# Optimization experiments

Hardware: AMD Instinct MI355X
Metric: run time of the kernel (lower is better)

Reference implementation:

```python
import jax, jax.numpy as jnp
import numpy as np

B, L, NE, DOUT = 4, 4096, 64, 64
DI = 128          # backbone model dim (hardcoded d_inner in MambaDoc)
NL = 2            # num_layers
H = 2             # num_heads
N = 128           # state_dim
G = 1             # num_groups
CONV = 4          # conv_size
DIN = 2 * DI      # expand=2 -> 256 inner channels of the mixer
P = DIN // H      # headdim = 128
CCH = DIN + 2 * G * N      # 512 conv channels (x, B, C)
DPROJ = 2 * DIN + 2 * G * N + H  # 770 in_proj output width


def setup_inputs() -> dict:
    key = jax.random.key(0)
    ks = jax.random.split(key, 8)
    s = lambda k, shape, sc: (jax.random.normal(k, shape, jnp.float32) * sc)
    return {
        "x": s(ks[0], (B, L, NE), 1.0),
        "in_w": s(ks[1], (DI, NE), (1.0 / NE) ** 0.5),
        "in_b": jnp.zeros((DI,), jnp.float32),
        "out_w": s(ks[2], (DOUT, DI), (1.0 / DI) ** 0.5),
        "out_b": jnp.zeros((DOUT,), jnp.float32),
        "l_rms_w": jnp.ones((NL, DI), jnp.float32),
        "l_in_w": s(ks[3], (NL, DPROJ, DI), (1.0 / DI) ** 0.5),
        "conv_w": s(ks[4], (NL, CCH, CONV), (1.0 / CONV) ** 0.5),
        "conv_b": jnp.zeros((NL, CCH), jnp.float32),
        "dt_bias": s(ks[5], (NL, H), 0.1),
        "A_log": jnp.zeros((NL, H), jnp.float32),   # A = -exp(A_log) = -1
        "D_p": jnp.ones((NL, H), jnp.float32),
        "gnorm_w": jnp.ones((NL, DIN), jnp.float32),
        "l_out_w": s(ks[6], (NL, DI, DIN), (1.0 / DIN) ** 0.5),
        "fnorm_w": jnp.ones((DI,), jnp.float32),
    }


def _rms(x, w, eps=1e-5):
    return x * jax.lax.rsqrt(jnp.mean(x * x, -1, keepdims=True) + eps) * w


def _mamba_layer(x, rms_w, in_w, cw, cb, dtb, a_log, d, gnw, ow):
    # x: (B,L,DI)
    h = _rms(x, rms_w)
    zxbcdt = jnp.einsum("bld,ed->ble", h, in_w)  # (B,L,770)
    z, xBC, dt = jnp.split(zxbcdt, [DIN, DIN + CCH], axis=-1)
    # causal depthwise conv over time, conv_size taps
    xp = jnp.pad(xBC, ((0, 0), (CONV - 1, 0), (0, 0)))
    xc = cb + sum(xp[:, k:k + L, :] * cw[:, k] for k in range(CONV))
    xc = jax.nn.silu(xc)
    xs, Bm, Cm = jnp.split(xc, [DIN, DIN + G * N], axis=-1)
    xs = xs.reshape(B, L, H, P)
    dt = jax.nn.softplus(dt + dtb)                 # (B,L,H)
    dA = jnp.exp(dt * (-jnp.exp(a_log)))           # (B,L,H) discrete decay

    def step(hc, inp):
        dA_t, dt_t, x_t, B_t, C_t = inp  # (B,H),(B,H),(B,H,P),(B,N),(B,N)
        hc = hc * dA_t[:, :, None, None] + (dt_t[:, :, None] * x_t)[..., None] * B_t[:, None, None, :]
        y = jnp.einsum("bhpn,bn->bhp", hc, C_t)
        return hc, y

    h0 = jnp.zeros((B, H, P, N), x.dtype)
    seq = (jnp.moveaxis(dA, 1, 0), jnp.moveaxis(dt, 1, 0), jnp.moveaxis(xs, 1, 0),
           jnp.moveaxis(Bm, 1, 0), jnp.moveaxis(Cm, 1, 0))
    _, ys = jax.lax.scan(step, h0, seq)
    y = jnp.moveaxis(ys, 0, 1)                     # (B,L,H,P)
    y = y + xs * d[None, None, :, None]            # D skip connection
    y = _rms(y.reshape(B, L, DIN) * jax.nn.silu(z), gnw)  # gated RMSNorm
    return x + jnp.einsum("ble,de->bld", y, ow)


def reference(x, in_w, in_b, out_w, out_b, l_rms_w, l_in_w, conv_w, conv_b,
              dt_bias, A_log, D_p, gnorm_w, l_out_w, fnorm_w):
    xp = jnp.einsum("bln,dn->bld", x, in_w) + in_b
    h = xp
    for i in range(NL):
        h = _mamba_layer(h, l_rms_w[i], l_in_w[i], conv_w[i], conv_b[i],
                         dt_bias[i], A_log[i], D_p[i], gnorm_w[i], l_out_w[i])
    h = _rms(h, fnorm_w)            # backbone final norm
    out = xp + h                    # outer residual in MambaDoc.forward
    return jnp.einsum("bld,od->blo", out, out_w) + out_b
```

## Files before the change

### kernel.cpp

```cpp
#include <hip/hip_runtime.h>
#include <cstddef>
#include <cstdint>


#define LSEQ 4096
#define MTOK 16384

typedef unsigned short u16;
typedef _Float16 f16x8 __attribute__((ext_vector_type(8)));
typedef float f32x4 __attribute__((ext_vector_type(4)));

__device__ __forceinline__ u16 f2h(float x) {
    return __builtin_bit_cast(u16, (_Float16)x);
}
__device__ __forceinline__ float h2f(u16 u) {
    return (float)__builtin_bit_cast(_Float16, u);
}
__device__ __forceinline__ float silu_f(float x) { return x / (1.f + __expf(-x)); }

__device__ __forceinline__ void async_lds16(const void* g, void* l) {
    __builtin_amdgcn_global_load_lds(
        (const __attribute__((address_space(1))) unsigned int*)g,
        (__attribute__((address_space(3))) unsigned int*)l, 16, 0, 0);
}

__device__ __forceinline__ uint4 cvt8(const float* __restrict__ src) {
    float4 a = *(const float4*)src;
    float4 b = *(const float4*)(src + 4);
    union { u16 u[8]; uint4 q; } pk;
    pk.u[0] = f2h(a.x); pk.u[1] = f2h(a.y); pk.u[2] = f2h(a.z); pk.u[3] = f2h(a.w);
    pk.u[4] = f2h(b.x); pk.u[5] = f2h(b.y); pk.u[6] = f2h(b.z); pk.u[7] = f2h(b.w);
    return pk.q;
}

__global__ __launch_bounds__(256) void gemm_rms0_kernel(
    const float* __restrict__ xf, const float* __restrict__ wf,
    const float* __restrict__ bias, const float* __restrict__ rmsw,
    u16* __restrict__ xp16, u16* __restrict__ hbuf16, u16* __restrict__ hn16)
{
    __shared__ u16 sA[64 * 64];
    __shared__ u16 sW[128 * 64];
    __shared__ float red[64][33];
    __shared__ float srstd[64];
    const int m0 = blockIdx.y * 64;
    const int tid = threadIdx.x, wid = tid >> 6, lane = tid & 63;
    const int wm = (wid >> 1) * 32, wn = (wid & 1) * 64;
    const int quad = lane >> 4, cl = lane & 15;
    #pragma unroll
    for (int i = 0; i < 2; i++) {
        int ck = i * 256 + tid;
        int r = ck >> 3, cc = ck & 7;
        int csw = (cc ^ (r & 7)) << 3;
        *(uint4*)&sA[ck * 8] = cvt8(xf + (size_t)(m0 + r) * 64 + csw);
    }
    #pragma unroll
    for (int i = 0; i < 4; i++) {
        int ck = i * 256 + tid;
        int r = ck >> 3, cc = ck & 7;
        int csw = (cc ^ (r & 7)) << 3;
        *(uint4*)&sW[ck * 8] = cvt8(wf + (size_t)r * 64 + csw);
    }
    __syncthreads();
    f32x4 acc[2][4];
    #pragma unroll
    for (int i = 0; i < 2; i++)
        #pragma unroll
        for (int j = 0; j < 4; j++) acc[i][j] = f32x4{0.f, 0.f, 0.f, 0.f};
    #pragma unroll
    for (int ks = 0; ks < 2; ks++) {
        f16x8 af[2], wv[4];
        int kc = ks * 4 + quad;
        #pragma unroll
        for (int i = 0; i < 2; i++) {
            int r = wm + i * 16 + cl;
            af[i] = *(const f16x8*)&sA[r * 64 + ((kc ^ (r & 7)) << 3)];
        }
        #pragma unroll
        for (int j = 0; j < 4; j++) {
            int r = wn + j * 16 + cl;
            wv[j] = *(const f16x8*)&sW[r * 64 + ((kc ^ (r & 7)) << 3)];
        }
        #pragma unroll
        for (int i = 0; i < 2; i++)
            #pragma unroll
            for (int j = 0; j < 4; j++)
                acc[i][j] = __builtin_amdgcn_mfma_f32_16x16x32_f16(
                    af[i], wv[j], acc[i][j], 0, 0, 0);
    }
    const int slot = (wid & 1) * 16 + cl;
    #pragma unroll
    for (int i = 0; i < 2; i++)
        #pragma unroll
        for (int r = 0; r < 4; r++) {
            int t = wm + i * 16 + quad * 4 + r;
            float ssp = 0.f;
            #pragma unroll
            for (int j = 0; j < 4; j++) {
                int n = wn + j * 16 + cl;
                float v = acc[i][j][r] + bias[n];
                acc[i][j][r] = v;
                ssp += v * v;
            }
            red[t][slot] = ssp;
        }
    __syncthreads();
    if (tid < 64) {
        float s = 0.f;
        #pragma unroll
        for (int sl = 0; sl < 32; sl++) s += red[tid][sl];
        srstd[tid] = rsqrtf(s * (1.f / 128.f) + 1e-5f);
    }
    __syncthreads();
    #pragma unroll
    for (int i = 0; i < 2; i++)
        #pragma unroll
        for (int r = 0; r < 4; r++) {
            int t = wm + i * 16 + quad * 4 + r;
            size_t ob = (size_t)(m0 + t) * 128;
            float rstd = srstd[t];
            #pragma unroll
            for (int j = 0; j < 4; j++) {
                int n = wn + j * 16 + cl;
                float v = acc[i][j][r];
                u16 vh = f2h(v);
                xp16[ob + n] = vh;
                hbuf16[ob + n] = vh;
                hn16[ob + n] = f2h(v * rstd * rmsw[n]);
            }
        }
}

__global__ __launch_bounds__(256) void gemm_inproj_kernel(
    const u16* __restrict__ A, const float* __restrict__ Wf,
    u16* __restrict__ zx16, float* __restrict__ dtb, float* __restrict__ Sb,
    const float* __restrict__ dt_bias, const float* __restrict__ A_log)
{
    __shared__ u16 sA[128 * 64];
    __shared__ u16 sW[128 * 64];
    __shared__ float sdt[2][128];
    const int K = 128, N = 770;
    const int n0 = blockIdx.x * 128, m0 = blockIdx.y * 128;
    const int tid = threadIdx.x, wid = tid >> 6, lane = tid & 63;
    const int wm = (wid >> 1) * 64, wn = (wid & 1) * 64;
    const int quad = lane >> 4, cl = lane & 15;
    f32x4 acc[4][4];
    #pragma unroll
    for (int i = 0; i < 4; i++)
        #pragma unroll
        for (int j = 0; j < 4; j++) acc[i][j] = f32x4{0.f, 0.f, 0.f, 0.f};

    for (int k0 = 0; k0 < K; k0 += 64) {
        #pragma unroll
        for (int i = 0; i < 4; i++) {
            int ck = i * 256 + tid;
            int r = ck >> 3, cc = ck & 7;
            int csw = (cc ^ (r & 7)) << 3;
            async_lds16(A + (size_t)(m0 + r) * K + k0 + csw,
                        (void*)(sA + (i * 256 + (tid & ~63)) * 8));
        }
        #pragma unroll
        for (int i = 0; i < 4; i++) {
            int ck = i * 256 + tid;
            int r = ck >> 3, cc = ck & 7;
            int csw = (cc ^ (r & 7)) << 3;
            int rr = n0 + r; if (rr >= N) rr = N - 1;
            *(uint4*)&sW[ck * 8] = cvt8(Wf + (size_t)rr * K + k0 + csw);
        }
        __syncthreads();
        #pragma unroll
        for (int ks = 0; ks < 2; ks++) {
            f16x8 af[4], wv[4];
            int kc = ks * 4 + quad;
            #pragma unroll
            for (int i = 0; i < 4; i++) {
                int r = wm + i * 16 + cl;
                af[i] = *(const f16x8*)&sA[r * 64 + ((kc ^ (r & 7)) << 3)];
            }
            #pragma unroll
            for (int j = 0; j < 4; j++) {
                int r = wn + j * 16 + cl;
                wv[j] = *(const f16x8*)&sW[r * 64 + ((kc ^ (r & 7)) << 3)];
            }
            #pragma unroll
            for (int i = 0; i < 4; i++)
                #pragma unroll
                for (int j = 0; j < 4; j++)
                    acc[i][j] = __builtin_amdgcn_mfma_f32_16x16x32_f16(
                        af[i], wv[j], acc[i][j], 0, 0, 0);
        }
        __syncthreads();
    }
    if (blockIdx.x < 6) {
        #pragma unroll
        for (int i = 0; i < 4; i++) {
            int m = m0 + wm + i * 16 + quad * 4;
            #pragma unroll
            for (int j = 0; j < 4; j++) {
                int n = n0 + wn + j * 16 + cl;
                #pragma unroll
                for (int r = 0; r < 4; r++)
                    zx16[(size_t)(m + r) * 768 + n] = f2h(acc[i][j][r]);
            }
        }
    } else {
        if ((wid & 1) == 0 && cl < 2) {
            #pragma unroll
            for (int i = 0; i < 4; i++)
                #pragma unroll
                for (int r = 0; r < 4; r++)
                    sdt[cl][wm + i * 16 + quad * 4 + r] = acc[i][0][r];
        }
        __syncthreads();
        const int hh = tid >> 7, t = tid & 127;
        float raw = sdt[hh][t] + dt_bias[hh];
        float dt = fmaxf(raw, 0.f) + log1pf(__expf(-fabsf(raw)));
        dtb[(size_t)(m0 + t) * 2 + hh] = dt;
        float ad = -__expf(A_log[hh]) * dt;
        __syncthreads();
        sdt[hh][t] = ad;
        __syncthreads();
        for (int off = 1; off < 128; off <<= 1) {
            float add = (t >= off) ? sdt[hh][t - off] : 0.f;
            __syncthreads();
            sdt[hh][t] += add;
            __syncthreads();
        }
        Sb[(size_t)(m0 + t) * 2 + hh] = sdt[hh][t];
    }
}

__global__ __launch_bounds__(512) void chunkstate_conv_kernel(
    const u16* __restrict__ zx16, const float* __restrict__ cw,
    const float* __restrict__ cb, const float* __restrict__ dtb,
    const float* __restrict__ Sb, u16* __restrict__ xT, u16* __restrict__ Hb)
{
    __shared__ u16 raw[2560 * 8];
    __shared__ u16 XT[128 * 128];
    __shared__ u16 BT[128 * 128];
    __shared__ float scw[2][128][4];
    __shared__ float scb[2][128];
    __shared__ float ssw[128];
    const int c = blockIdx.x, h = blockIdx.y, b = blockIdx.z;
    const int tid = threadIdx.x, wid = tid >> 6, lane = tid & 63;
    const int quad = lane >> 4, cl = lane & 15;
    const int tok0 = b * LSEQ + c * 128;
    for (int idx = tid; idx < 256; idx += 512) {
        int grp = idx >> 7, j = idx & 127;
        int ch = grp ? (256 + j) : (128 * h + j);
        float4 w4 = *(const float4*)&cw[ch * 4];
        scw[grp][j][0] = w4.x; scw[grp][j][1] = w4.y;
        scw[grp][j][2] = w4.z; scw[grp][j][3] = w4.w;
        scb[grp][j] = cb[ch];
    }
    if (tid < 128) {
        float Sl = Sb[(size_t)(tok0 + 127) * 2 + h];
        ssw[tid] = __expf(Sl - Sb[(size_t)(tok0 + tid) * 2 + h])
                   * dtb[(size_t)(tok0 + tid) * 2 + h];
    }
    #pragma unroll
    for (int i = 0; i < 5; i++) {
        int ck = i * 512 + tid;
        int r = ck >> 4; if (r > 130) r = 130;
        int cc = ck & 15;
        int tok = tok0 - 3 + r; if (tok < 0) tok = 0;
        async_lds16(zx16 + (size_t)tok * 768 + 256 + 128 * h + ((cc ^ (r & 15)) << 3),
                    (void*)(raw + (i * 512 + (tid & ~63)) * 8));
    }
    __syncthreads();
    if (c == 0 && tid < 48) *(uint4*)&raw[tid * 8] = make_uint4(0, 0, 0, 0);
    __syncthreads();
    #pragma unroll
    for (int it = 0; it < 4; it++) {
        int idx = it * 512 + tid;
        int s = idx & 127, pg = idx >> 7;
        f16x8 v[4];
        #pragma unroll
        for (int k = 0; k < 4; k++) {
            int rr = s + k;
            v[k] = *(const f16x8*)&raw[rr * 128 + ((pg ^ (rr & 15)) << 3)];
        }
        #pragma unroll
        for (int j = 0; j < 8; j++) {
            int p = pg * 8 + j;
            float o = scb[0][p] + (float)v[0][j] * scw[0][p][0]
                    + (float)v[1][j] * scw[0][p][1]
                    + (float)v[2][j] * scw[0][p][2]
                    + (float)v[3][j] * scw[0][p][3];
            o = silu_f(o);
            XT[p * 128 + (((s >> 3) ^ (p & 15)) << 3) + (s & 7)] = f2h(o);
        }
    }
    __syncthreads();
    const size_t blk = ((size_t)((b * 2 + h) * 32 + c)) << 14;
    #pragma unroll
    for (int i = 0; i < 5; i++) {
        int ck = i * 512 + tid;
        int r = ck >> 4; if (r > 130) r = 130;
        int cc = ck & 15;
        int tok = tok0 - 3 + r; if (tok < 0) tok = 0;
        async_lds16(zx16 + (size_t)tok * 768 + 512 + ((cc ^ (r & 15)) << 3),
                    (void*)(raw + (i * 512 + (tid & ~63)) * 8));
    }
    #pragma unroll
    for (int it = 0; it < 4; it++) {
        int ck = it * 512 + tid;
        int r = ck >> 4, cc = ck & 15;
        uint4 q = *(const uint4*)&XT[r * 128 + ((cc ^ (r & 15)) << 3)];
        *(uint4*)&xT[blk + (size_t)r * 128 + cc * 8] = q;
    }
    __syncthreads();
    if (c == 0 && tid < 48) *(uint4*)&raw[tid * 8] = make_uint4(0, 0, 0, 0);
    __syncthreads();
    #pragma unroll
    for (int it = 0; it < 4; it++) {
        int idx = it * 512 + tid;
        int s = idx & 127, ng = idx >> 7;
        f16x8 v[4];
        #pragma unroll
        for (int k = 0; k < 4; k++) {
            int rr = s + k;
            v[k] = *(const f16x8*)&raw[rr * 128 + ((ng ^ (rr & 15)) << 3)];
        }
        float wsv = ssw[s];
        #pragma unroll
        for (int j = 0; j < 8; j++) {
            int n = ng * 8 + j;
            float o = scb[1][n] + (float)v[0][j] * scw[1][n][0]
                    + (float)v[1][j] * scw[1][n][1]
                    + (float)v[2][j] * scw[1][n][2]
                    + (float)v[3][j] * scw[1][n][3];
            o = silu_f(o) * wsv;
            BT[n * 128 + (((s >> 3) ^ (n & 15)) << 3) + (s & 7)] = f2h(o);
        }
    }
    __syncthreads();
    const int wm = (wid >> 1) * 32, wn = (wid & 1) * 64;
    f32x4 acc[2][4];
    #pragma unroll
    for (int i = 0; i < 2; i++)
        #pragma unroll
        for (int j = 0; j < 4; j++) acc[i][j] = f32x4{0.f, 0.f, 0.f, 0.f};
    #pragma unroll
    for (int ks = 0; ks < 4; ks++) {
        f16x8 xa[2], bb[4];
        int kc = ks * 4 + quad;
        #pragma unroll
        for (int i = 0; i < 2; i++) {
            int r = wm + i * 16 + cl;
            xa[i] = *(const f16x8*)&XT[r * 128 + ((kc ^ (r & 15)) << 3)];
        }
        #pragma unroll
        for (int j = 0; j < 4; j++) {
            int r = wn + j * 16 + cl;
            bb[j] = *(const f16x8*)&BT[r * 128 + ((kc ^ (r & 15)) << 3)];
        }
        #pragma unroll
        for (int i = 0; i < 2; i++)
            #pragma unroll
            for (int j = 0; j < 4; j++)
                acc[i][j] = __builtin_amdgcn_mfma_f32_16x16x32_f16(
                    xa[i], bb[j], acc[i][j], 0, 0, 0);
    }
    u16* out = Hb + blk;
    #pragma unroll
    for (int i = 0; i < 2; i++)
        #pragma unroll
        for (int j = 0; j < 4; j++)
            #pragma unroll
            for (int r = 0; r < 4; r++)
                out[(size_t)(wm + i * 16 + quad * 4 + r) * 128 + wn + j * 16 + cl]
                    = f2h(acc[i][j][r]);
}

__global__ __launch_bounds__(256) void statecombine_kernel(
    const float* __restrict__ Sb, const u16* __restrict__ Hb,
    u16* __restrict__ Hbf)
{
    const int e = blockIdx.x * 256 + threadIdx.x;
    const int h = blockIdx.y, b = blockIdx.z;
    const size_t base = ((size_t)((b * 2 + h) * 32)) << 14;
    float state = 0.f;
    for (int c = 0; c < 32; c++) {
        size_t idx = base + ((size_t)c << 14) + e;
        float v = h2f(Hb[idx]);
        Hbf[idx] = f2h(state);
        float dec = __expf(Sb[(size_t)(b * LSEQ + c * 128 + 127) * 2 + h]);
        state = dec * state + v;
    }
}

__global__ __launch_bounds__(512) void ssd_fused_conv_kernel(
    const u16* __restrict__ zx16, const u16* __restrict__ xT,
    const u16* __restrict__ Hbf, const float* __restrict__ dtb,
    const float* __restrict__ Sb, const float* __restrict__ cw,
    const float* __restrict__ cb, const float* __restrict__ gnw,
    const float* __restrict__ Dp, u16* __restrict__ y16)
{
    __shared__ u16 bufCW[2][128 * 128];
    __shared__ u16 bufH[2][128 * 128];
    __shared__ float sS[2][128], sdt[2][128];
    __shared__ float scw2[2][128][4];
    __shared__ float scb2[2][128];
    __shared__ float red[128][5];
    __shared__ float srstd[128];
    const int c = blockIdx.x, b = blockIdx.y;
    const int tid = threadIdx.x, wid = tid >> 6, lane = tid & 63;
    const int quad = lane >> 4, cl = lane & 15;
    const int tok0 = b * LSEQ + c * 128;
    const size_t blk0 = ((size_t)((b * 2 + 0) * 32 + c)) << 14;
    const size_t blk1 = ((size_t)((b * 2 + 1) * 32 + c)) << 14;
    u16* scratch = &bufH[0][0];
    for (int idx = tid; idx < 256; idx += 512) {
        int grp = idx >> 7, j = idx & 127;
        int ch = grp ? (256 + j) : (384 + j);
        float4 w4 = *(const float4*)&cw[ch * 4];
        scw2[grp][j][0] = w4.x; scw2[grp][j][1] = w4.y;
        scw2[grp][j][2] = w4.z; scw2[grp][j][3] = w4.w;
        scb2[grp][j] = cb[ch];
    }
    if (tid < 256) {
        int hh = tid >> 7, t = tid & 127;
        sS[hh][t] = Sb[(size_t)(tok0 + t) * 2 + hh];
        sdt[hh][t] = dtb[(size_t)(tok0 + t) * 2 + hh];
    }
    #pragma unroll
    for (int i = 0; i < 5; i++) {
        int ck = i * 512 + tid;
        int r = ck >> 4; if (r > 130) r = 130;
        int cc = ck & 15;
        int tok = tok0 - 3 + r; if (tok < 0) tok = 0;
        async_lds16(zx16 + (size_t)tok * 768 + 640 + ((cc ^ (r & 15)) << 3),
                    (void*)(scratch + (i * 512 + (tid & ~63)) * 8));
    }
    __syncthreads();
    if (c == 0 && tid < 48) *(uint4*)&scratch[tid * 8] = make_uint4(0, 0, 0, 0);
    __syncthreads();
    #pragma unroll
    for (int it = 0; it < 4; it++) {
        int idx = it * 512 + tid;
        int t = idx & 127, ng = idx >> 7;
        f16x8 v[4];
        #pragma unroll
        for (int k = 0; k < 4; k++) {
            int rr = t + k;
            v[k] = *(const f16x8*)&scratch[rr * 128 + ((ng ^ (rr & 15)) << 3)];
        }
        union { u16 u[8]; uint4 q; } pk;
        #pragma unroll
        for (int j = 0; j < 8; j++) {
            int n = ng * 8 + j;
            float o = scb2[0][n] + (float)v[0][j] * scw2[0][n][0]
                    + (float)v[1][j] * scw2[0][n][1]
                    + (float)v[2][j] * scw2[0][n][2]
                    + (float)v[3][j] * scw2[0][n][3];
            pk.u[j] = f2h(silu_f(o));
        }
        *(uint4*)&bufCW[0][t * 128 + ((ng ^ (t & 15)) << 3)] = pk.q;
    }
    __syncthreads();
    #pragma unroll
    for (int i = 0; i < 5; i++) {
        int ck = i * 512 + tid;
        int r = ck >> 4; if (r > 130) r = 130;
        int cc = ck & 15;
        int tok = tok0 - 3 + r; if (tok < 0) tok = 0;
        async_lds16(zx16 + (size_t)tok * 768 + 512 + ((cc ^ (r & 15)) << 3),
                    (void*)(scratch + (i * 512 + (tid & ~63)) * 8));
    }
    __syncthreads();
    if (c == 0 && tid < 48) *(uint4*)&scratch[tid * 8] = make_uint4(0, 0, 0, 0);
    __syncthreads();
    #pragma unroll
    for (int it = 0; it < 4; it++) {
        int idx = it * 512 + tid;
        int t = idx & 127, ng = idx >> 7;
        f16x8 v[4];
        #pragma unroll
        for (int k = 0; k < 4; k++) {
            int rr = t + k;
            v[k] = *(const f16x8*)&scratch[rr * 128 + ((ng ^ (rr & 15)) << 3)];
        }
        union { u16 u[8]; uint4 q; } pk;
        #pragma unroll
        for (int j = 0; j < 8; j++) {
            int n = ng * 8 + j;
            float o = scb2[1][n] + (float)v[0][j] * scw2[1][n][0]
                    + (float)v[1][j] * scw2[1][n][1]
                    + (float)v[2][j] * scw2[1][n][2]
                    + (float)v[3][j] * scw2[1][n][3];
            pk.u[j] = f2h(silu_f(o));
        }
        *(uint4*)&bufCW[1][t * 128 + ((ng ^ (t & 15)) << 3)] = pk.q;
    }
    __syncthreads();
    #pragma unroll
    for (int i = 0; i < 4; i++) {
        int ck = i * 512 + tid;
        int r = ck >> 4, cc = ck & 15;
        int csw = (cc ^ (r & 15)) << 3;
        int ldst = (i * 512 + (tid & ~63)) * 8;
        async_lds16(Hbf + blk0 + (size_t)r * 128 + csw, (void*)(&bufH[0][0] + ldst));
        async_lds16(Hbf + blk1 + (size_t)r * 128 + csw, (void*)(&bufH[1][0] + ldst));
    }
    __syncthreads();
    const int h = wid >> 2, w2 = wid & 3;
    const int wm = (w2 >> 1) * 64, wn = (w2 & 1) * 64;
    f32x4 acc[4][4];
    #pragma unroll
    for (int i = 0; i < 4; i++)
        #pragma unroll
        for (int j = 0; j < 4; j++) acc[i][j] = f32x4{0.f, 0.f, 0.f, 0.f};
    #pragma unroll
    for (int ks = 0; ks < 4; ks++) {
        f16x8 ca[4], hb[4];
        int kc = ks * 4 + quad;
        #pragma unroll
        for (int i = 0; i < 4; i++) {
            int r = wm + i * 16 + cl;
            ca[i] = *(const f16x8*)&bufCW[0][r * 128 + ((kc ^ (r & 15)) << 3)];
        }
        #pragma unroll
        for (int j = 0; j < 4; j++) {
            int r = wn + j * 16 + cl;
            hb[j] = *(const f16x8*)&bufH[h][r * 128 + ((kc ^ (r & 15)) << 3)];
        }
        #pragma unroll
        for (int i = 0; i < 4; i++)
            #pragma unroll
            for (int j = 0; j < 4; j++)
                acc[i][j] = __builtin_amdgcn_mfma_f32_16x16x32_f16(
                    ca[i], hb[j], acc[i][j], 0, 0, 0);
    }
    #pragma unroll
    for (int i = 0; i < 4; i++)
        #pragma unroll
        for (int r = 0; r < 4; r++) {
            float e = __expf(sS[h][wm + i * 16 + quad * 4 + r]);
            #pragma unroll
            for (int j = 0; j < 4; j++) acc[i][j][r] *= e;
        }
    const int sm0 = (wid >> 1) * 32, sn0 = (wid & 1) * 64;
    f32x4 sacc[2][4];
    #pragma unroll
    for (int i = 0; i < 2; i++)
        #pragma unroll
        for (int j = 0; j < 4; j++) sacc[i][j] = f32x4{0.f, 0.f, 0.f, 0.f};
    #pragma unroll
    for (int ks = 0; ks < 4; ks++) {
        f16x8 cs[2], bs[4];
        int kc = ks * 4 + quad;
        #pragma unroll
        for (int i2 = 0; i2 < 2; i2++) {
            int r = sm0 + i2 * 16 + cl;
            cs[i2] = *(const f16x8*)&bufCW[0][r * 128 + ((kc ^ (r & 15)) << 3)];
        }
        #pragma unroll
        for (int j = 0; j < 4; j++) {
            int r = sn0 + j * 16 + cl;
            bs[j] = *(const f16x8*)&bufCW[1][r * 128 + ((kc ^ (r & 15)) << 3)];
        }
        #pragma unroll
        for (int i2 = 0; i2 < 2; i2++)
            #pragma unroll
            for (int j = 0; j < 4; j++)
                if (sm0 + i2 * 16 + 15 >= sn0 + j * 16)
                    sacc[i2][j] = __builtin_amdgcn_mfma_f32_16x16x32_f16(
                        cs[i2], bs[j], sacc[i2][j], 0, 0, 0);
    }
    __syncthreads();
    #pragma unroll
    for (int i = 0; i < 4; i++) {
        int ck = i * 512 + tid;
        int r = ck >> 4, cc = ck & 15;
        int csw = (cc ^ (r & 15)) << 3;
        int ldst = (i * 512 + (tid & ~63)) * 8;
        async_lds16(xT + blk0 + (size_t)r * 128 + csw, (void*)(&bufH[0][0] + ldst));
        async_lds16(xT + blk1 + (size_t)r * 128 + csw, (void*)(&bufH[1][0] + ldst));
    }
    #pragma unroll
    for (int hh = 0; hh < 2; hh++)
        #pragma unroll
        for (int i2 = 0; i2 < 2; i2++)
            #pragma unroll
            for (int r = 0; r < 4; r++) {
                int t = sm0 + i2 * 16 + quad * 4 + r;
                float Stv = sS[hh][t];
                #pragma unroll
                for (int j = 0; j < 4; j++) {
                    int s = sn0 + j * 16 + cl;
                    float gv = 0.f;
                    if (s <= t)
                        gv = sacc[i2][j][r] * __expf(Stv - sS[hh][s]) * sdt[hh][s];
                    bufCW[hh][t * 128 + (((s >> 3) ^ (t & 15)) << 3) + (s & 7)] = f2h(gv);
                }
            }
    __syncthreads();
    #pragma unroll
    for (int ks = 0; ks < 4; ks++) {
        f16x8 ga[4], xb[4];
        int kc = ks * 4 + quad;
        #pragma unroll
        for (int i = 0; i < 4; i++) {
            int r = wm + i * 16 + cl;
            ga[i] = *(const f16x8*)&bufCW[h][r * 128 + ((kc ^ (r & 15)) << 3)];
        }
        #pragma unroll
        for (int j = 0; j < 4; j++) {
            int r = wn + j * 16 + cl;
            xb[j] = *(const f16x8*)&bufH[h][r * 128 + ((kc ^ (r & 15)) << 3)];
        }
        #pragma unroll
        for (int i = 0; i < 4; i++)
            #pragma unroll
            for (int j = 0; j < 4; j++)
                acc[i][j] = __builtin_amdgcn_mfma_f32_16x16x32_f16(
                    ga[i], xb[j], acc[i][j], 0, 0, 0);
    }
    const float dco = Dp[h];
    #pragma unroll
    for (int i = 0; i < 4; i++)
        #pragma unroll
        for (int r = 0; r < 4; r++) {
            int t = wm + i * 16 + quad * 4 + r;
            float ssp = 0.f;
            #pragma unroll
            for (int j = 0; j < 4; j++) {
                int p = wn + j * 16 + cl;
                float xv = h2f(bufH[h][p * 128 + (((t >> 3) ^ (p & 15)) << 3) + (t & 7)]);
                float zv = h2f(zx16[(size_t)(tok0 + t) * 768 + h * 128 + p]);
                float g = (acc[i][j][r] + dco * xv) * silu_f(zv);
                acc[i][j][r] = g;
                ssp += g * g;
            }
            ssp += __shfl_xor(ssp, 1);
            ssp += __shfl_xor(ssp, 2);
            ssp += __shfl_xor(ssp, 4);
            ssp += __shfl_xor(ssp, 8);
            if (cl == 0) red[t][h * 2 + (wn >> 6)] = ssp;
        }
    __syncthreads();
    if (tid < 128)
        srstd[tid] = rsqrtf((red[tid][0] + red[tid][1] + red[tid][2] + red[tid][3])
                            * (1.f / 256.f) + 1e-5f);
    __syncthreads();
    #pragma unroll
    for (int i = 0; i < 4; i++)
        #pragma unroll
        for (int r = 0; r < 4; r++) {
            int t = wm + i * 16 + quad * 4 + r;
            float rstd = srstd[t];
            u16* row = y16 + (size_t)(tok0 + t) * 256;
            #pragma unroll
            for (int j = 0; j < 4; j++) {
                int p = wn + j * 16 + cl;
                int e = h * 128 + p;
                row[e] = f2h(acc[i][j][r] * rstd * gnw[e]);
            }
        }
}

__global__ __launch_bounds__(256) void gemm_outrms_kernel(
    const u16* __restrict__ A, const float* __restrict__ Wf,
    const float* __restrict__ rmsw, u16* __restrict__ xp16,
    u16* __restrict__ hbuf16, u16* __restrict__ hn16,
    const float* __restrict__ out_wf, const float* __restrict__ out_b,
    float* __restrict__ dout, int mode)
{
    __shared__ u16 sA[64 * 64];
    __shared__ u16 sW[128 * 64];
    __shared__ float red[64][33];
    __shared__ float srstd[64];
    __shared__ u16 hn2[64 * 128];
    __shared__ u16 ow[64 * 128];
    const int K = 256;
    const int m0 = blockIdx.y * 64;
    const int tid = threadIdx.x, wid = tid >> 6, lane = tid & 63;
    const int wm = (wid >> 1) * 32, wn = (wid & 1) * 64;
    const int quad = lane >> 4, cl = lane & 15;
    f32x4 acc[2][4];
    #pragma unroll
    for (int i = 0; i < 2; i++)
        #pragma unroll
        for (int j = 0; j < 4; j++) acc[i][j] = f32x4{0.f, 0.f, 0.f, 0.f};

    for (int k0 = 0; k0 < K; k0 += 64) {
        #pragma unroll
        for (int i = 0; i < 2; i++) {
            int ck = i * 256 + tid;
            int r = ck >> 3, cc = ck & 7;
            int csw = (cc ^ (r & 7)) << 3;
            async_lds16(A + (size_t)(m0 + r) * K + k0 + csw,
                        (void*)(sA + (i * 256 + (tid & ~63)) * 8));
        }
        #pragma unroll
        for (int i = 0; i < 4; i++) {
            int ck = i * 256 + tid;
            int r = ck >> 3, cc = ck & 7;
            int csw = (cc ^ (r & 7)) << 3;
            *(uint4*)&sW[ck * 8] = cvt8(Wf + (size_t)r * K + k0 + csw);
        }
        __syncthreads();
        #pragma unroll
        for (int ks = 0; ks < 2; ks++) {
            f16x8 af[2], wv[4];
            int kc = ks * 4 + quad;
            #pragma unroll
            for (int i = 0; i < 2; i++) {
                int r = wm + i * 16 + cl;
                af[i] = *(const f16x8*)&sA[r * 64 + ((kc ^ (r & 7)) << 3)];
            }
            #pragma unroll
            for (int j = 0; j < 4; j++) {
                int r = wn + j * 16 + cl;
                wv[j] = *(const f16x8*)&sW[r * 64 + ((kc ^ (r & 7)) << 3)];
            }
            #pragma unroll
            for (int i = 0; i < 2; i++)
                #pragma unroll
                for (int j = 0; j < 4; j++)
                    acc[i][j] = __builtin_amdgcn_mfma_f32_16x16x32_f16(
                        af[i], wv[j], acc[i][j], 0, 0, 0);
        }
        __syncthreads();
    }
    const int slot = (wid & 1) * 16 + cl;
    #pragma unroll
    for (int i = 0; i < 2; i++)
        #pragma unroll
        for (int r = 0; r < 4; r++) {
            int t = wm + i * 16 + quad * 4 + r;
            size_t ob = (size_t)(m0 + t) * 128;
            float ssp = 0.f;
            #pragma unroll
            for (int j = 0; j < 4; j++) {
                int n = wn + j * 16 + cl;
                float v = acc[i][j][r] + h2f(hbuf16[ob + n]);
                acc[i][j][r] = v;
                ssp += v * v;
            }
            red[t][slot] = ssp;
        }
    __syncthreads();
    if (tid < 64) {
        float s = 0.f;
        #pragma unroll
        for (int sl = 0; sl < 32; sl++) s += red[tid][sl];
        srstd[tid] = rsqrtf(s * (1.f / 128.f) + 1e-5f);
    }
    __syncthreads();
    #pragma unroll
    for (int i = 0; i < 2; i++)
        #pragma unroll
        for (int r = 0; r < 4; r++) {
            int t = wm + i * 16 + quad * 4 + r;
            size_t ob = (size_t)(m0 + t) * 128;
            float rstd = srstd[t];
            #pragma unroll
            for (int j = 0; j < 4; j++) {
                int n = wn + j * 16 + cl;
                float v = acc[i][j][r];
                float val = v * rstd * rmsw[n];
                if (mode == 1) {
                    hbuf16[ob + n] = f2h(v);
                    hn16[ob + n] = f2h(val);
                } else {
                    val += h2f(xp16[ob + n]);
                    hn2[t * 128 + (((n >> 3) ^ (t & 15)) << 3) + (n & 7)] = f2h(val);
                }
            }
        }
    if (mode == 1) return;
    #pragma unroll
    for (int i = 0; i < 4; i++) {
        int ck = i * 256 + tid;
        int rr = ck >> 4, cc = ck & 15;
        int csw = (cc ^ (rr & 15)) << 3;
        *(uint4*)&ow[ck * 8] = cvt8(out_wf + (size_t)rr * 128 + csw);
    }
    __syncthreads();
    const int wm4 = (wid >> 1) * 32, wn4 = (wid & 1) * 32;
    f32x4 acc2[2][2];
    #pragma unroll
    for (int i = 0; i < 2; i++)
        #pragma unroll
        for (int j = 0; j < 2; j++) acc2[i][j] = f32x4{0.f, 0.f, 0.f, 0.f};
    #pragma unroll
    for (int ks = 0; ks < 4; ks++) {
        f16x8 af2[2], wf2[2];
        int kc = ks * 4 + quad;
        #pragma unroll
        for (int i = 0; i < 2; i++) {
            int r = wm4 + i * 16 + cl;
            af2[i] = *(const f16x8*)&hn2[r * 128 + ((kc ^ (r & 15)) << 3)];
        }
        #pragma unroll
        for (int j = 0; j < 2; j++) {
            int rr = wn4 + j * 16 + cl;
            wf2[j] = *(const f16x8*)&ow[rr * 128 + ((kc ^ (rr & 15)) << 3)];
        }
        #pragma unroll
        for (int i = 0; i < 2; i++)
            #pragma unroll
            for (int j = 0; j < 2; j++)
                acc2[i][j] = __builtin_amdgcn_mfma_f32_16x16x32_f16(
                    af2[i], wf2[j], acc2[i][j], 0, 0, 0);
    }
    #pragma unroll
    for (int i = 0; i < 2; i++) {
        int m = m0 + wm4 + i * 16 + quad * 4;
        #pragma unroll
        for (int j = 0; j < 2; j++) {
            int n = wn4 + j * 16 + cl;
            float bv = out_b[n];
            #pragma unroll
            for (int r = 0; r < 4; r++)
                dout[(size_t)(m + r) * 64 + n] = acc2[i][j][r] + bv;
        }
    }
}

extern "C" void kernel_launch(void* const* d_in, const int* in_sizes, int n_in,
                              void* d_out, int out_size, void* d_ws, size_t ws_size,
                              hipStream_t stream)
{
    (void)in_sizes; (void)n_in; (void)out_size; (void)ws_size;
    const float* x       = (const float*)d_in[0];
    const float* in_w    = (const float*)d_in[1];
    const float* in_b    = (const float*)d_in[2];
    const float* out_w   = (const float*)d_in[3];
    const float* out_b   = (const float*)d_in[4];
    const float* l_rms_w = (const float*)d_in[5];
    const float* l_in_w  = (const float*)d_in[6];
    const float* conv_w  = (const float*)d_in[7];
    const float* conv_b  = (const float*)d_in[8];
    const float* dt_bias = (const float*)d_in[9];
    const float* A_log   = (const float*)d_in[10];
    const float* D_p     = (const float*)d_in[11];
    const float* gnorm_w = (const float*)d_in[12];
    const float* l_out_w = (const float*)d_in[13];
    const float* fnorm_w = (const float*)d_in[14];

    char* w = (char*)d_ws;
    u16*   xp16   = (u16*)(w);
    u16*   hbuf16 = (u16*)(w + 4194304);
    u16*   hn16   = (u16*)(w + 8388608);
    u16*   zx16   = (u16*)(w + 12582912);
    float* dtb    = (float*)(w + 37748736);
    float* Sb     = (float*)(w + 37879808);
    u16*   Hb     = (u16*)(w + 38010880);
    u16*   Hbf    = (u16*)(w + 46399488);
    u16*   xT     = (u16*)(w + 54788096);
    u16*   y16    = (u16*)(w + 63176704);

    gemm_rms0_kernel<<<dim3(1, 256), 256, 0, stream>>>(
        x, in_w, in_b, l_rms_w, xp16, hbuf16, hn16);

    for (int i = 0; i < 2; i++) {
        gemm_inproj_kernel<<<dim3(7, 128), 256, 0, stream>>>(
            hn16, l_in_w + (size_t)i * 770 * 128, zx16, dtb, Sb,
            dt_bias + i * 2, A_log + i * 2);
        chunkstate_conv_kernel<<<dim3(32, 2, 4), 512, 0, stream>>>(
            zx16, conv_w + i * 2048, conv_b + i * 512, dtb, Sb, xT, Hb);
        statecombine_kernel<<<dim3(64, 2, 4), 256, 0, stream>>>(Sb, Hb, Hbf);
        ssd_fused_conv_kernel<<<dim3(32, 4), 512, 0, stream>>>(
            zx16, xT, Hbf, dtb, Sb, conv_w + i * 2048, conv_b + i * 512,
            gnorm_w + i * 256, D_p + i * 2, y16);
        gemm_outrms_kernel<<<dim3(1, 256), 256, 0, stream>>>(
            y16, l_out_w + (size_t)i * 128 * 256,
            (i == 0) ? (l_rms_w + 128) : fnorm_w, xp16, hbuf16, hn16,
            out_w, out_b, (float*)d_out, (i == 0) ? 1 : 3);
    }
}
```

Measured before the change: 246.2 us.

## Split SSD kernel per head and move gated RMSNorm into out-proj GEMM

The SSD output kernel now launches one block per (chunk, head, batch) instead of per (chunk, batch), which doubles the grid to 256 blocks. Each block recomputes the x-channel conv for its own head instead of reading a stored xT buffer, so the chunkstate kernel no longer writes xT. Because a single block no longer holds both heads, the cross-head gated RMSNorm moves into the out-projection GEMM. That kernel first computes the per-row rstd from the un-normalized gated output, folds gnorm_w into the weight conversion, and scales the accumulator by rstd. The trade is extra conv recomputation and an extra pass over the 256-wide row in the out GEMM, in exchange for more parallelism and less global traffic.

```diff
diff --git a/kernel.cpp b/kernel.cpp
--- a/kernel.cpp
+++ b/kernel.cpp
@@ -30,6 +30,20 @@
     union { u16 u[8]; uint4 q; } pk;
     pk.u[0] = f2h(a.x); pk.u[1] = f2h(a.y); pk.u[2] = f2h(a.z); pk.u[3] = f2h(a.w);
     pk.u[4] = f2h(b.x); pk.u[5] = f2h(b.y); pk.u[6] = f2h(b.z); pk.u[7] = f2h(b.w);
+    return pk.q;
+}
+
+__device__ __forceinline__ uint4 cvt8g(const float* __restrict__ src,
+                                       const float* __restrict__ gw) {
+    float4 a = *(const float4*)src;
+    float4 b = *(const float4*)(src + 4);
+    float4 ga = *(const float4*)gw;
+    float4 gb = *(const float4*)(gw + 4);
+    union { u16 u[8]; uint4 q; } pk;
+    pk.u[0] = f2h(a.x * ga.x); pk.u[1] = f2h(a.y * ga.y);
+    pk.u[2] = f2h(a.z * ga.z); pk.u[3] = f2h(a.w * ga.w);
+    pk.u[4] = f2h(b.x * gb.x); pk.u[5] = f2h(b.y * gb.y);
+    pk.u[6] = f2h(b.z * gb.z); pk.u[7] = f2h(b.w * gb.w);
     return pk.q;
 }
 
@@ -232,7 +246,7 @@
 __global__ __launch_bounds__(512) void chunkstate_conv_kernel(
     const u16* __restrict__ zx16, const float* __restrict__ cw,
     const float* __restrict__ cb, const float* __restrict__ dtb,
-    const float* __restrict__ Sb, u16* __restrict__ xT, u16* __restrict__ Hb)
+    const float* __restrict__ Sb, u16* __restrict__ Hb)
 {
     __shared__ u16 raw[2560 * 8];
     __shared__ u16 XT[128 * 128];
@@ -291,7 +305,6 @@
         }
     }
     __syncthreads();
-    const size_t blk = ((size_t)((b * 2 + h) * 32 + c)) << 14;
     #pragma unroll
     for (int i = 0; i < 5; i++) {
         int ck = i * 512 + tid;
@@ -300,13 +313,6 @@
         int tok = tok0 - 3 + r; if (tok < 0) tok = 0;
         async_lds16(zx16 + (size_t)tok * 768 + 512 + ((cc ^ (r & 15)) << 3),
                     (void*)(raw + (i * 512 + (tid & ~63)) * 8));
-    }
-    #pragma unroll
-    for (int it = 0; it < 4; it++) {
-        int ck = it * 512 + tid;
-        int r = ck >> 4, cc = ck & 15;
-        uint4 q = *(const uint4*)&XT[r * 128 + ((cc ^ (r & 15)) << 3)];
-        *(uint4*)&xT[blk + (size_t)r * 128 + cc * 8] = q;
     }
     __syncthreads();
     if (c == 0 && tid < 48) *(uint4*)&raw[tid * 8] = make_uint4(0, 0, 0, 0);
@@ -334,6 +340,7 @@
         }
     }
     __syncthreads();
+    const size_t blk = ((size_t)((b * 2 + h) * 32 + c)) << 14;
     const int wm = (wid >> 1) * 32, wn = (wid & 1) * 64;
     f32x4 acc[2][4];
     #pragma unroll
@@ -389,40 +396,104 @@
     }
 }
 
-__global__ __launch_bounds__(512) void ssd_fused_conv_kernel(
-    const u16* __restrict__ zx16, const u16* __restrict__ xT,
-    const u16* __restrict__ Hbf, const float* __restrict__ dtb,
-    const float* __restrict__ Sb, const float* __restrict__ cw,
-    const float* __restrict__ cb, const float* __restrict__ gnw,
-    const float* __restrict__ Dp, u16* __restrict__ y16)
+__global__ __launch_bounds__(512) void ssd_ph_kernel(
+    const u16* __restrict__ zx16, const u16* __restrict__ Hbf,
+    const float* __restrict__ dtb, const float* __restrict__ Sb,
+    const float* __restrict__ cw, const float* __restrict__ cb,
+    const float* __restrict__ Dp, u16* __restrict__ g16)
 {
-    __shared__ u16 bufCW[2][128 * 128];
-    __shared__ u16 bufH[2][128 * 128];
-    __shared__ float sS[2][128], sdt[2][128];
-    __shared__ float scw2[2][128][4];
-    __shared__ float scb2[2][128];
-    __shared__ float red[128][5];
-    __shared__ float srstd[128];
-    const int c = blockIdx.x, b = blockIdx.y;
+    __shared__ u16 raw[2560 * 8];
+    __shared__ u16 XT[128 * 128];
+    __shared__ u16 Btok[128 * 128];
+    __shared__ u16 Ctok[128 * 128];
+    __shared__ float sS[128], sdt[128];
+    __shared__ float scw[3][128][4];
+    __shared__ float scb[3][128];
+    const int c = blockIdx.x, h = blockIdx.y, b = blockIdx.z;
     const int tid = threadIdx.x, wid = tid >> 6, lane = tid & 63;
     const int quad = lane >> 4, cl = lane & 15;
     const int tok0 = b * LSEQ + c * 128;
-    const size_t blk0 = ((size_t)((b * 2 + 0) * 32 + c)) << 14;
-    const size_t blk1 = ((size_t)((b * 2 + 1) * 32 + c)) << 14;
-    u16* scratch = &bufH[0][0];
-    for (int idx = tid; idx < 256; idx += 512) {
+    const size_t blk = ((size_t)((b * 2 + h) * 32 + c)) << 14;
+    for (int idx = tid; idx < 384; idx += 512) {
         int grp = idx >> 7, j = idx & 127;
-        int ch = grp ? (256 + j) : (384 + j);
+        int ch = (grp == 0) ? (128 * h + j) : (grp == 1 ? 256 + j : 384 + j);
         float4 w4 = *(const float4*)&cw[ch * 4];
-        scw2[grp][j][0] = w4.x; scw2[grp][j][1] = w4.y;
-        scw2[grp][j][2] = w4.z; scw2[grp][j][3] = w4.w;
-        scb2[grp][j] = cb[ch];
-    }
-    if (tid < 256) {
-        int hh = tid >> 7, t = tid & 127;
-        sS[hh][t] = Sb[(size_t)(tok0 + t) * 2 + hh];
-        sdt[hh][t] = dtb[(size_t)(tok0 + t) * 2 + hh];
-    }
+        scw[grp][j][0] = w4.x; scw[grp][j][1] = w4.y;
+        scw[grp][j][2] = w4.z; scw[grp][j][3] = w4.w;
+        scb[grp][j] = cb[ch];
+    }
+    if (tid < 128) {
+        sS[tid] = Sb[(size_t)(tok0 + tid) * 2 + h];
+        sdt[tid] = dtb[(size_t)(tok0 + tid) * 2 + h];
+    }
+    #pragma unroll
+    for (int i = 0; i < 5; i++) {
+        int ck = i * 512 + tid;
+        int r = ck >> 4; if (r > 130) r = 130;
+        int cc = ck & 15;
+        int tok = tok0 - 3 + r; if (tok < 0) tok = 0;
+        async_lds16(zx16 + (size_t)tok * 768 + 256 + 128 * h + ((cc ^ (r & 15)) << 3),
+                    (void*)(raw + (i * 512 + (tid & ~63)) * 8));
+    }
+    __syncthreads();
+    if (c == 0 && tid < 48) *(uint4*)&raw[tid * 8] = make_uint4(0, 0, 0, 0);
+    __syncthreads();
+    #pragma unroll
+    for (int it = 0; it < 4; it++) {
+        int idx = it * 512 + tid;
+        int s = idx & 127, pg = idx >> 7;
+        f16x8 v[4];
+        #pragma unroll
+        for (int k = 0; k < 4; k++) {
+            int rr = s + k;
+            v[k] = *(const f16x8*)&raw[rr * 128 + ((pg ^ (rr & 15)) << 3)];
+        }
+        #pragma unroll
+        for (int j = 0; j < 8; j++) {
+            int p = pg * 8 + j;
+            float o = scb[0][p] + (float)v[0][j] * scw[0][p][0]
+                    + (float)v[1][j] * scw[0][p][1]
+                    + (float)v[2][j] * scw[0][p][2]
+                    + (float)v[3][j] * scw[0][p][3];
+            XT[p * 128 + (((s >> 3) ^ (p & 15)) << 3) + (s & 7)] = f2h(silu_f(o));
+        }
+    }
+    __syncthreads();
+    #pragma unroll
+    for (int i = 0; i < 5; i++) {
+        int ck = i * 512 + tid;
+        int r = ck >> 4; if (r > 130) r = 130;
+        int cc = ck & 15;
+        int tok = tok0 - 3 + r; if (tok < 0) tok = 0;
+        async_lds16(zx16 + (size_t)tok * 768 + 512 + ((cc ^ (r & 15)) << 3),
+                    (void*)(raw + (i * 512 + (tid & ~63)) * 8));
+    }
+    __syncthreads();
+    if (c == 0 && tid < 48) *(uint4*)&raw[tid * 8] = make_uint4(0, 0, 0, 0);
+    __syncthreads();
+    #pragma unroll
+    for (int it = 0; it < 4; it++) {
+        int idx = it * 512 + tid;
+        int t = idx & 127, ng = idx >> 7;
+        f16x8 v[4];
+        #pragma unroll
+        for (int k = 0; k < 4; k++) {
+            int rr = t + k;
+            v[k] = *(const f16x8*)&raw[rr * 128 + ((ng ^ (rr & 15)) << 3)];
+        }
+        union { u16 u[8]; uint4 q; } pk;
+        #pragma unroll
+        for (int j = 0; j < 8; j++) {
+            int n = ng * 8 + j;
+            float o = scb[1][n] + (float)v[0][j] * scw[1][n][0]
+                    + (float)v[1][j] * scw[1][n][1]
+                    + (float)v[2][j] * scw[1][n][2]
+                    + (float)v[3][j] * scw[1][n][3];
+            pk.u[j] = f2h(silu_f(o));
+        }
+        *(uint4*)&Btok[t * 128 + ((ng ^ (t & 15)) << 3)] = pk.q;
+    }
+    __syncthreads();
     #pragma unroll
     for (int i = 0; i < 5; i++) {
         int ck = i * 512 + tid;
@@ -430,10 +501,10 @@
         int cc = ck & 15;
         int tok = tok0 - 3 + r; if (tok < 0) tok = 0;
         async_lds16(zx16 + (size_t)tok * 768 + 640 + ((cc ^ (r & 15)) << 3),
-                    (void*)(scratch + (i * 512 + (tid & ~63)) * 8));
-    }
-    __syncthreads();
-    if (c == 0 && tid < 48) *(uint4*)&scratch[tid * 8] = make_uint4(0, 0, 0, 0);
+                    (void*)(raw + (i * 512 + (tid & ~63)) * 8));
+    }
+    __syncthreads();
+    if (c == 0 && tid < 48) *(uint4*)&raw[tid * 8] = make_uint4(0, 0, 0, 0);
     __syncthreads();
     #pragma unroll
     for (int it = 0; it < 4; it++) {
@@ -443,103 +514,64 @@
         #pragma unroll
         for (int k = 0; k < 4; k++) {
             int rr = t + k;
-            v[k] = *(const f16x8*)&scratch[rr * 128 + ((ng ^ (rr & 15)) << 3)];
+            v[k] = *(const f16x8*)&raw[rr * 128 + ((ng ^ (rr & 15)) << 3)];
         }
         union { u16 u[8]; uint4 q; } pk;
         #pragma unroll
         for (int j = 0; j < 8; j++) {
             int n = ng * 8 + j;
-            float o = scb2[0][n] + (float)v[0][j] * scw2[0][n][0]
-                    + (float)v[1][j] * scw2[0][n][1]
-                    + (float)v[2][j] * scw2[0][n][2]
-                    + (float)v[3][j] * scw2[0][n][3];
+            float o = scb[2][n] + (float)v[0][j] * scw[2][n][0]
+                    + (float)v[1][j] * scw[2][n][1]
+                    + (float)v[2][j] * scw[2][n][2]
+                    + (float)v[3][j] * scw[2][n][3];
             pk.u[j] = f2h(silu_f(o));
         }
-        *(uint4*)&bufCW[0][t * 128 + ((ng ^ (t & 15)) << 3)] = pk.q;
-    }
-    __syncthreads();
-    #pragma unroll
-    for (int i = 0; i < 5; i++) {
-        int ck = i * 512 + tid;
-        int r = ck >> 4; if (r > 130) r = 130;
-        int cc = ck & 15;
-        int tok = tok0 - 3 + r; if (tok < 0) tok = 0;
-        async_lds16(zx16 + (size_t)tok * 768 + 512 + ((cc ^ (r & 15)) << 3),
-                    (void*)(scratch + (i * 512 + (tid & ~63)) * 8));
-    }
-    __syncthreads();
-    if (c == 0 && tid < 48) *(uint4*)&scratch[tid * 8] = make_uint4(0, 0, 0, 0);
-    __syncthreads();
-    #pragma unroll
-    for (int it = 0; it < 4; it++) {
-        int idx = it * 512 + tid;
-        int t = idx & 127, ng = idx >> 7;
-        f16x8 v[4];
-        #pragma unroll
-        for (int k = 0; k < 4; k++) {
-            int rr = t + k;
-            v[k] = *(const f16x8*)&scratch[rr * 128 + ((ng ^ (rr & 15)) << 3)];
-        }
-        union { u16 u[8]; uint4 q; } pk;
-        #pragma unroll
-        for (int j = 0; j < 8; j++) {
-            int n = ng * 8 + j;
-            float o = scb2[1][n] + (float)v[0][j] * scw2[1][n][0]
-                    + (float)v[1][j] * scw2[1][n][1]
-                    + (float)v[2][j] * scw2[1][n][2]
-                    + (float)v[3][j] * scw2[1][n][3];
-            pk.u[j] = f2h(silu_f(o));
-        }
-        *(uint4*)&bufCW[1][t * 128 + ((ng ^ (t & 15)) << 3)] = pk.q;
+        *(uint4*)&Ctok[t * 128 + ((ng ^ (t & 15)) << 3)] = pk.q;
     }
     __syncthreads();
     #pragma unroll
     for (int i = 0; i < 4; i++) {
         int ck = i * 512 + tid;
         int r = ck >> 4, cc = ck & 15;
-        int csw = (cc ^ (r & 15)) << 3;
-        int ldst = (i * 512 + (tid & ~63)) * 8;
-        async_lds16(Hbf + blk0 + (size_t)r * 128 + csw, (void*)(&bufH[0][0] + ldst));
-        async_lds16(Hbf + blk1 + (size_t)r * 128 + csw, (void*)(&bufH[1][0] + ldst));
-    }
-    __syncthreads();
-    const int h = wid >> 2, w2 = wid & 3;
-    const int wm = (w2 >> 1) * 64, wn = (w2 & 1) * 64;
-    f32x4 acc[4][4];
-    #pragma unroll
-    for (int i = 0; i < 4; i++)
+        async_lds16(Hbf + blk + (size_t)r * 128 + ((cc ^ (r & 15)) << 3),
+                    (void*)(raw + (i * 512 + (tid & ~63)) * 8));
+    }
+    __syncthreads();
+    const int wm = (wid >> 1) * 32, wn = (wid & 1) * 64;
+    f32x4 acc[2][4];
+    #pragma unroll
+    for (int i = 0; i < 2; i++)
         #pragma unroll
         for (int j = 0; j < 4; j++) acc[i][j] = f32x4{0.f, 0.f, 0.f, 0.f};
     #pragma unroll
     for (int ks = 0; ks < 4; ks++) {
-        f16x8 ca[4], hb[4];
+        f16x8 ca[2], hb[4];
         int kc = ks * 4 + quad;
         #pragma unroll
-        for (int i = 0; i < 4; i++) {
+        for (int i = 0; i < 2; i++) {
             int r = wm + i * 16 + cl;
-            ca[i] = *(const f16x8*)&bufCW[0][r * 128 + ((kc ^ (r & 15)) << 3)];
+            ca[i] = *(const f16x8*)&Ctok[r * 128 + ((kc ^ (r & 15)) << 3)];
         }
         #pragma unroll
         for (int j = 0; j < 4; j++) {
             int r = wn + j * 16 + cl;
-            hb[j] = *(const f16x8*)&bufH[h][r * 128 + ((kc ^ (r & 15)) << 3)];
-        }
-        #pragma unroll
-        for (int i = 0; i < 4; i++)
+            hb[j] = *(const f16x8*)&raw[r * 128 + ((kc ^ (r & 15)) << 3)];
+        }
+        #pragma unroll
+        for (int i = 0; i < 2; i++)
             #pragma unroll
             for (int j = 0; j < 4; j++)
                 acc[i][j] = __builtin_amdgcn_mfma_f32_16x16x32_f16(
                     ca[i], hb[j], acc[i][j], 0, 0, 0);
     }
     #pragma unroll
-    for (int i = 0; i < 4; i++)
+    for (int i = 0; i < 2; i++)
         #pragma unroll
         for (int r = 0; r < 4; r++) {
-            float e = __expf(sS[h][wm + i * 16 + quad * 4 + r]);
+            float e = __expf(sS[wm + i * 16 + quad * 4 + r]);
             #pragma unroll
             for (int j = 0; j < 4; j++) acc[i][j][r] *= e;
         }
-    const int sm0 = (wid >> 1) * 32, sn0 = (wid & 1) * 64;
     f32x4 sacc[2][4];
     #pragma unroll
     for (int i = 0; i < 2; i++)
@@ -551,66 +583,54 @@
         int kc = ks * 4 + quad;
         #pragma unroll
         for (int i2 = 0; i2 < 2; i2++) {
-            int r = sm0 + i2 * 16 + cl;
-            cs[i2] = *(const f16x8*)&bufCW[0][r * 128 + ((kc ^ (r & 15)) << 3)];
+            int r = wm + i2 * 16 + cl;
+            cs[i2] = *(const f16x8*)&Ctok[r * 128 + ((kc ^ (r & 15)) << 3)];
         }
         #pragma unroll
         for (int j = 0; j < 4; j++) {
-            int r = sn0 + j * 16 + cl;
-            bs[j] = *(const f16x8*)&bufCW[1][r * 128 + ((kc ^ (r & 15)) << 3)];
+            int r = wn + j * 16 + cl;
+            bs[j] = *(const f16x8*)&Btok[r * 128 + ((kc ^ (r & 15)) << 3)];
         }
         #pragma unroll
         for (int i2 = 0; i2 < 2; i2++)
             #pragma unroll
             for (int j = 0; j < 4; j++)
-                if (sm0 + i2 * 16 + 15 >= sn0 + j * 16)
+                if (wm + i2 * 16 + 15 >= wn + j * 16)
                     sacc[i2][j] = __builtin_amdgcn_mfma_f32_16x16x32_f16(
                         cs[i2], bs[j], sacc[i2][j], 0, 0, 0);
     }
     __syncthreads();
     #pragma unroll
-    for (int i = 0; i < 4; i++) {
-        int ck = i * 512 + tid;
-        int r = ck >> 4, cc = ck & 15;
-        int csw = (cc ^ (r & 15)) << 3;
-        int ldst = (i * 512 + (tid & ~63)) * 8;
-        async_lds16(xT + blk0 + (size_t)r * 128 + csw, (void*)(&bufH[0][0] + ldst));
-        async_lds16(xT + blk1 + (size_t)r * 128 + csw, (void*)(&bufH[1][0] + ldst));
-    }
-    #pragma unroll
-    for (int hh = 0; hh < 2; hh++)
-        #pragma unroll
-        for (int i2 = 0; i2 < 2; i2++)
-            #pragma unroll
-            for (int r = 0; r < 4; r++) {
-                int t = sm0 + i2 * 16 + quad * 4 + r;
-                float Stv = sS[hh][t];
-                #pragma unroll
-                for (int j = 0; j < 4; j++) {
-                    int s = sn0 + j * 16 + cl;
-                    float gv = 0.f;
-                    if (s <= t)
-                        gv = sacc[i2][j][r] * __expf(Stv - sS[hh][s]) * sdt[hh][s];
-                    bufCW[hh][t * 128 + (((s >> 3) ^ (t & 15)) << 3) + (s & 7)] = f2h(gv);
-                }
-            }
+    for (int i2 = 0; i2 < 2; i2++)
+        #pragma unroll
+        for (int r = 0; r < 4; r++) {
+            int t = wm + i2 * 16 + quad * 4 + r;
+            float Stv = sS[t];
+            #pragma unroll
+            for (int j = 0; j < 4; j++) {
+                int s = wn + j * 16 + cl;
+                float gv = 0.f;
+                if (s <= t) gv = sacc[i2][j][r] * __expf(Stv - sS[s]) * sdt[s];
+                raw[t * 128 + (((s >> 3) ^ (t & 15)) << 3) + (s & 7)] = f2h(gv);
+            }
+        }
     __syncthreads();
     #pragma unroll
     for (int ks = 0; ks < 4; ks++) {
-        f16x8 ga[4], xb[4];
+        f16x8 ga[2], xb[4];
         int kc = ks * 4 + quad;
         #pragma unroll
-        for (int i = 0; i < 4; i++) {
+        for (int i = 0; i < 2; i++) {
             int r = wm + i * 16 + cl;
-            ga[i] = *(const f16x8*)&bufCW[h][r * 128 + ((kc ^ (r & 15)) << 3)];
+            ga[i] = *(const f16x8*)&raw[r * 128 + ((kc ^ (r & 15)) << 3)];
         }
         #pragma unroll
         for (int j = 0; j < 4; j++) {
             int r = wn + j * 16 + cl;
-            xb[j] = *(const f16x8*)&bufH[h][r * 128 + ((kc ^ (r & 15)) << 3)];
-        }
-        #pragma unroll
-        for (int i = 0; i < 4; i++)
+            xb[j] = *(const f16x8*)&XT[r * 128 + ((kc ^ (r & 15)) << 3)];
+        }
+        #pragma unroll
+        for (int i = 0; i < 2; i++)
             #pragma unroll
             for (int j = 0; j < 4; j++)
                 acc[i][j] = __builtin_amdgcn_mfma_f32_16x16x32_f16(
@@ -618,51 +638,25 @@
     }
     const float dco = Dp[h];
     #pragma unroll
-    for (int i = 0; i < 4; i++)
+    for (int i = 0; i < 2; i++)
         #pragma unroll
         for (int r = 0; r < 4; r++) {
             int t = wm + i * 16 + quad * 4 + r;
-            float ssp = 0.f;
+            u16* row = g16 + (size_t)(tok0 + t) * 256 + h * 128;
             #pragma unroll
             for (int j = 0; j < 4; j++) {
                 int p = wn + j * 16 + cl;
-                float xv = h2f(bufH[h][p * 128 + (((t >> 3) ^ (p & 15)) << 3) + (t & 7)]);
+                float xv = h2f(XT[p * 128 + (((t >> 3) ^ (p & 15)) << 3) + (t & 7)]);
                 float zv = h2f(zx16[(size_t)(tok0 + t) * 768 + h * 128 + p]);
-                float g = (acc[i][j][r] + dco * xv) * silu_f(zv);
-                acc[i][j][r] = g;
-                ssp += g * g;
-            }
-            ssp += __shfl_xor(ssp, 1);
-            ssp += __shfl_xor(ssp, 2);
-            ssp += __shfl_xor(ssp, 4);
-            ssp += __shfl_xor(ssp, 8);
-            if (cl == 0) red[t][h * 2 + (wn >> 6)] = ssp;
-        }
-    __syncthreads();
-    if (tid < 128)
-        srstd[tid] = rsqrtf((red[tid][0] + red[tid][1] + red[tid][2] + red[tid][3])
-                            * (1.f / 256.f) + 1e-5f);
-    __syncthreads();
-    #pragma unroll
-    for (int i = 0; i < 4; i++)
-        #pragma unroll
-        for (int r = 0; r < 4; r++) {
-            int t = wm + i * 16 + quad * 4 + r;
-            float rstd = srstd[t];
-            u16* row = y16 + (size_t)(tok0 + t) * 256;
-            #pragma unroll
-            for (int j = 0; j < 4; j++) {
-                int p = wn + j * 16 + cl;
-                int e = h * 128 + p;
-                row[e] = f2h(acc[i][j][r] * rstd * gnw[e]);
+                row[p] = f2h((acc[i][j][r] + dco * xv) * silu_f(zv));
             }
         }
 }
 
 __global__ __launch_bounds__(256) void gemm_outrms_kernel(
     const u16* __restrict__ A, const float* __restrict__ Wf,
-    const float* __restrict__ rmsw, u16* __restrict__ xp16,
-    u16* __restrict__ hbuf16, u16* __restrict__ hn16,
+    const float* __restrict__ gnw, const float* __restrict__ rmsw,
+    u16* __restrict__ xp16, u16* __restrict__ hbuf16, u16* __restrict__ hn16,
     const float* __restrict__ out_wf, const float* __restrict__ out_b,
     float* __restrict__ dout, int mode)
 {
@@ -670,6 +664,8 @@
     __shared__ u16 sW[128 * 64];
     __shared__ float red[64][33];
     __shared__ float srstd[64];
+    __shared__ float redp[64][5];
+    __shared__ float rstdg[64];
     __shared__ u16 hn2[64 * 128];
     __shared__ u16 ow[64 * 128];
     const int K = 256;
@@ -677,6 +673,22 @@
     const int tid = threadIdx.x, wid = tid >> 6, lane = tid & 63;
     const int wm = (wid >> 1) * 32, wn = (wid & 1) * 64;
     const int quad = lane >> 4, cl = lane & 15;
+    {
+        int t = tid >> 2, q = tid & 3;
+        const u16* row = A + (size_t)(m0 + t) * 256 + q * 64;
+        float ss = 0.f;
+        #pragma unroll
+        for (int u = 0; u < 8; u++) {
+            f16x8 v = *(const f16x8*)&row[u * 8];
+            #pragma unroll
+            for (int j = 0; j < 8; j++) { float f = (float)v[j]; ss += f * f; }
+        }
+        redp[t][q] = ss;
+    }
+    __syncthreads();
+    if (tid < 64)
+        rstdg[tid] = rsqrtf((redp[tid][0] + redp[tid][1] + redp[tid][2]
+                             + redp[tid][3]) * (1.f / 256.f) + 1e-5f);
     f32x4 acc[2][4];
     #pragma unroll
     for (int i = 0; i < 2; i++)
@@ -697,7 +709,8 @@
             int ck = i * 256 + tid;
             int r = ck >> 3, cc = ck & 7;
             int csw = (cc ^ (r & 7)) << 3;
-            *(uint4*)&sW[ck * 8] = cvt8(Wf + (size_t)r * K + k0 + csw);
+            *(uint4*)&sW[ck * 8] = cvt8g(Wf + (size_t)r * K + k0 + csw,
+                                         gnw + k0 + csw);
         }
         __syncthreads();
         #pragma unroll
@@ -730,11 +743,12 @@
         for (int r = 0; r < 4; r++) {
             int t = wm + i * 16 + quad * 4 + r;
             size_t ob = (size_t)(m0 + t) * 128;
+            float rg = rstdg[t];
             float ssp = 0.f;
             #pragma unroll
             for (int j = 0; j < 4; j++) {
                 int n = wn + j * 16 + cl;
-                float v = acc[i][j][r] + h2f(hbuf16[ob + n]);
+                float v = acc[i][j][r] * rg + h2f(hbuf16[ob + n]);
                 acc[i][j][r] = v;
                 ssp += v * v;
             }
@@ -849,8 +863,7 @@
     float* Sb     = (float*)(w + 37879808);
     u16*   Hb     = (u16*)(w + 38010880);
     u16*   Hbf    = (u16*)(w + 46399488);
-    u16*   xT     = (u16*)(w + 54788096);
-    u16*   y16    = (u16*)(w + 63176704);
+    u16*   g16    = (u16*)(w + 54788096);
 
     gemm_rms0_kernel<<<dim3(1, 256), 256, 0, stream>>>(
         x, in_w, in_b, l_rms_w, xp16, hbuf16, hn16);
@@ -860,13 +873,13 @@
             hn16, l_in_w + (size_t)i * 770 * 128, zx16, dtb, Sb,
             dt_bias + i * 2, A_log + i * 2);
         chunkstate_conv_kernel<<<dim3(32, 2, 4), 512, 0, stream>>>(
-            zx16, conv_w + i * 2048, conv_b + i * 512, dtb, Sb, xT, Hb);
+            zx16, conv_w + i * 2048, conv_b + i * 512, dtb, Sb, Hb);
         statecombine_kernel<<<dim3(64, 2, 4), 256, 0, stream>>>(Sb, Hb, Hbf);
-        ssd_fused_conv_kernel<<<dim3(32, 4), 512, 0, stream>>>(
-            zx16, xT, Hbf, dtb, Sb, conv_w + i * 2048, conv_b + i * 512,
-            gnorm_w + i * 256, D_p + i * 2, y16);
+        ssd_ph_kernel<<<dim3(32, 2, 4), 512, 0, stream>>>(
+            zx16, Hbf, dtb, Sb, conv_w + i * 2048, conv_b + i * 512,
+            D_p + i * 2, g16);
         gemm_outrms_kernel<<<dim3(1, 256), 256, 0, stream>>>(
-            y16, l_out_w + (size_t)i * 128 * 256,
+            g16, l_out_w + (size_t)i * 128 * 256, gnorm_w + i * 256,
             (i == 0) ? (l_rms_w + 128) : fnorm_w, xp16, hbuf16, hn16,
             out_w, out_b, (float*)d_out, (i == 0) ? 1 : 3);
     }
```

After: 231.4 us. -6.0%, faster.
